# Kernel optimization log

Measured on AMD Instinct MI355X. Metric: run time of the kernel, lower is better.

The kernel has to match this reference:

```python
import jax, jax.numpy as jnp
import numpy as np

MID = 64        # conf.mid_channels
N_INV = 6       # n_layers=8 -> range(1, n_layers-1) -> 6 involution blocks
K = 7           # involution kernel size
GROUP_CH = 16   # RedNet default group_channels
GROUPS = MID // GROUP_CH   # 4
RED = MID // 4             # reduction_ratio = 4 -> 16


def conv2d(x, w, b=None, pad=0):
    out = jax.lax.conv_general_dilated(
        x, w, window_strides=(1, 1), padding=[(pad, pad), (pad, pad)],
        dimension_numbers=('NCHW', 'OIHW', 'NCHW'))
    if b is not None:
        out = out + b[None, :, None, None]
    return out


def extract_patches(x, k):
    # x: (B,C,H,W) -> (B,C,k*k,H,W), same-padded (torch nn.Unfold with pad=k//2)
    p = k // 2
    xp = jnp.pad(x, ((0, 0), (0, 0), (p, p), (p, p)))
    H, W = x.shape[2], x.shape[3]
    slices = [xp[:, :, i:i + H, j:j + W] for i in range(k) for j in range(k)]
    return jnp.stack(slices, axis=2)


def involution(x, red_w, bn_gamma, bn_beta, span_w, span_b):
    # kernel-generation branch: 1x1 conv (no bias) -> BN(eval, mean=0,var=1) -> ReLU -> 1x1 conv
    t = conv2d(x, red_w)                                     # (B,RED,H,W)
    t = bn_gamma[None, :, None, None] * t + bn_beta[None, :, None, None]
    t = jax.nn.relu(t)
    w = conv2d(t, span_w, span_b)                            # (B,K*K*GROUPS,H,W)
    B, _, H, W = w.shape
    w = w.reshape(B, GROUPS, K * K, H, W)
    patches = extract_patches(x, K).reshape(B, GROUPS, GROUP_CH, K * K, H, W)
    out = jnp.einsum('bgkhw,bgckhw->bgchw', w, patches)      # per-pixel dynamic conv
    return out.reshape(B, MID, H, W)


def setup_inputs() -> dict:
    key = jax.random.key(0)
    ks = jax.random.split(key, 12)
    s = 0.05
    inp = {
        'input_tensor': jax.random.normal(ks[0], (1, 3, 128, 128), jnp.float32),
        'conv_in_w': jax.random.normal(ks[1], (MID, 3, 3, 3), jnp.float32) * s,
        'conv_in_b': jax.random.normal(ks[2], (MID,), jnp.float32) * s,
        'red_w': jax.random.normal(ks[3], (N_INV, RED, MID, 1, 1), jnp.float32) * s,
        'bn_gamma': jnp.ones((N_INV, RED), jnp.float32),
        'bn_beta': jnp.zeros((N_INV, RED), jnp.float32),
        'span_w': jax.random.normal(ks[4], (N_INV, K * K * GROUPS, RED, 1, 1), jnp.float32) * s,
        'span_b': jax.random.normal(ks[5], (N_INV, K * K * GROUPS), jnp.float32) * s,
        'conv_out_w': jax.random.normal(ks[6], (12, MID, 3, 3), jnp.float32) * s,
        'conv_out_b': jax.random.normal(ks[7], (12,), jnp.float32) * s,
    }
    return inp


def reference(input_tensor, conv_in_w, conv_in_b, red_w, bn_gamma, bn_beta,
              span_w, span_b, conv_out_w, conv_out_b):
    x = conv2d(input_tensor, conv_in_w, conv_in_b, pad=2)     # (B,MID,H+2,W+2)
    for l in range(N_INV):
        x = jax.nn.relu(involution(x, red_w[l], bn_gamma[l], bn_beta[l],
                                   span_w[l], span_b[l]))
    pixel = conv2d(x, conv_out_w, conv_out_b, pad=0)          # (B,12,H,W)
    # PixelShuffle(2): (B,12,H,W) -> (B,3,2H,2W)
    B, _, H, W = pixel.shape
    out = pixel.reshape(B, 3, 2, 2, H, W).transpose(0, 1, 4, 2, 5, 3)
    return out.reshape(B, 3, 2 * H, 2 * W)
```

## Files before the change

kernel.cpp:

```cpp
#include <hip/hip_runtime.h>


#define HH 130
#define SP 136
#define PPL (SP*SP)
#define GP (PPL*16)
#define XBUF2 (4*GP)
#define TP1 (16900*16)
#define OFF_TA (2*XBUF2)
#define OFF_TB (OFF_TA + 4*TP1)

__global__ __launch_bounds__(256) void conv_in_kernel(
        const float* __restrict__ inf, const float* __restrict__ W,
        const float* __restrict__ b, float* __restrict__ x0,
        float* __restrict__ x1, float* __restrict__ tpA,
        const float* __restrict__ redw0) {
    const int tid = threadIdx.x;
    if (blockIdx.x >= 67) {
        int idx = ((blockIdx.x - 67)*4 + blockIdx.y)*256 + tid;
        if (idx < 3192) {
            int bsel = idx & 1, e = idx >> 1;
            int r, c;
            if (e < 816) { r = e/136; c = e%136; if (r >= 3) r += 130; }
            else { int j = e-816; r = 3 + j/6; int m = j%6; c = (m<3)? m : m+130; }
            float* base = (bsel ? x1 : x0) + ((size_t)r*SP + c)*16;
            float4 z = make_float4(0.f,0.f,0.f,0.f);
            #pragma unroll
            for (int g2 = 0; g2 < 4; ++g2)
                #pragma unroll
                for (int q = 0; q < 4; ++q)
                    *(float4*)(base + (size_t)g2*GP + q*4) = z;
        }
        return;
    }
    __shared__ float wl[448];
    const int g = blockIdx.y;
    for (int i = tid; i < 448; i += 256)
        wl[i] = (i < 432) ? W[g*432 + i] : b[g*16 + (i-432)];
    __syncthreads();
    int px = blockIdx.x*256 + tid;
    int pxc = px < 16900 ? px : 16899;
    int h = pxc/130, w = pxc%130;
    float xv[27];
    #pragma unroll
    for (int i = 0; i < 3; ++i)
      #pragma unroll
      for (int ky = 0; ky < 3; ++ky) {
        int y = h - 2 + ky;
        #pragma unroll
        for (int kx = 0; kx < 3; ++kx) {
            int xx = w - 2 + kx;
            float v = 0.f;
            if ((unsigned)y < 128u && (unsigned)xx < 128u)
                v = inf[i*16384 + y*128 + xx];
            xv[i*9 + ky*3 + kx] = v;
        }
      }
    float acc[16];
    #pragma unroll
    for (int c = 0; c < 16; ++c) {
        float a = wl[432 + c];
        #pragma unroll
        for (int t = 0; t < 27; ++t) a += wl[c*27 + t] * xv[t];
        acc[c] = a;
    }
    if (px < 16900) {
        float* dst = x0 + (size_t)g*GP + ((size_t)(h+3)*SP + (w+3))*16;
        #pragma unroll
        for (int q = 0; q < 4; ++q)
            *(float4*)(dst + q*4) =
                make_float4(acc[q*4], acc[q*4+1], acc[q*4+2], acc[q*4+3]);
        float* td = tpA + (size_t)g*TP1 + (size_t)px*16;
        #pragma unroll
        for (int rq = 0; rq < 4; ++rq) {
            float p0=0.f, p1=0.f, p2=0.f, p3=0.f;
            #pragma unroll
            for (int j = 0; j < 16; ++j) {
                float a = acc[j];
                p0 += redw0[(rq*4+0)*64 + g*16 + j]*a;
                p1 += redw0[(rq*4+1)*64 + g*16 + j]*a;
                p2 += redw0[(rq*4+2)*64 + g*16 + j]*a;
                p3 += redw0[(rq*4+3)*64 + g*16 + j]*a;
            }
            *(float4*)(td + rq*4) = make_float4(p0, p1, p2, p3);
        }
    }
}

#define TL(p, r)  uu[(p)*20 + (r)]
#define WLK(k, p) uu[(k)*68 + (p)]
__global__ __launch_bounds__(256, 5) void e_kernel(
        const float* __restrict__ x,
        const float* __restrict__ tread,
        float* __restrict__ twrite,
        const float* __restrict__ gamma, const float* __restrict__ beta,
        const float* __restrict__ spanw,
        const float* __restrict__ spanb,
        const float* __restrict__ redwn,
        float* __restrict__ xout,
        const int doNext)
{
    __shared__ float xl[4][14][17][4];
    __shared__ float uu[49*68];
    const int wid = blockIdx.x;
    const int slot = wid >> 3;
    const int T = (wid & 7)*37 + (slot >> 2);
    if (T >= 289) return;
    const int g = slot & 3;
    const int ty = (T/17)*8, tx = (T%17)*8;
    const int tid = threadIdx.x;
    const int px = tid & 63;
    const int wv = __builtin_amdgcn_readfirstlane(tid >> 6);
    const int sr = px >> 3, sc = px & 7;

    for (int i = tid; i < 784; i += 256) {
        int q = i & 3, p = i >> 2;
        int r = p / 14, c = p % 14;
        int gr = ty + r, gc = tx + c;
        gr = gr < SP ? gr : SP-1;
        gc = gc < SP ? gc : SP-1;
        float4 v = *(const float4*)(x + (size_t)g*GP
                                    + ((size_t)gr*SP + gc)*16 + q*4);
        *(float4*)&xl[q][r][c][0] = v;
    }

    const int hh = min(ty + sr, HH-1), ww = min(tx + sc, HH-1);
    {
        const size_t toff = ((size_t)hh*HH + ww)*16 + wv*4;
        float4 s = make_float4(0.f,0.f,0.f,0.f);
        #pragma unroll
        for (int gg = 0; gg < 4; ++gg) {
            float4 a = *(const float4*)(tread + (size_t)gg*TP1 + toff);
            s.x += a.x; s.y += a.y; s.z += a.z; s.w += a.w;
        }
        *(float4*)&TL(px, wv*4) = s;
    }
    __syncthreads();

    float t16[16];
    #pragma unroll
    for (int q = 0; q < 4; ++q) {
        float4 v = *(const float4*)&TL(px, q*4);
        t16[q*4+0] = fmaxf(gamma[q*4+0]*v.x + beta[q*4+0], 0.f);
        t16[q*4+1] = fmaxf(gamma[q*4+1]*v.y + beta[q*4+1], 0.f);
        t16[q*4+2] = fmaxf(gamma[q*4+2]*v.z + beta[q*4+2], 0.f);
        t16[q*4+3] = fmaxf(gamma[q*4+3]*v.w + beta[q*4+3], 0.f);
    }
    __syncthreads();

    {
        const float* sw = spanw + g*784;
        const float* sb = spanb + g*49;
        const int k0 = wv ? (wv*12 + 1) : 0;
        #pragma unroll
        for (int j = 0; j < 12; ++j) {
            int k = k0 + j;
            float a = sb[k];
            #pragma unroll
            for (int r = 0; r < 16; ++r) a += sw[k*16 + r] * t16[r];
            WLK(k, px) = a;
        }
        if (wv == 0) {
            float a = sb[12];
            #pragma unroll
            for (int r = 0; r < 16; ++r) a += sw[12*16 + r] * t16[r];
            WLK(12, px) = a;
        }
    }
    __syncthreads();

    float4 o0 = make_float4(0.f,0.f,0.f,0.f);
    float4 o1 = make_float4(0.f,0.f,0.f,0.f);
    int px0 = 0, cq2 = 0;
    if (tid < 128) {
        cq2 = tid >> 5;
        const int pr = tid & 31;
        const int sr2 = pr >> 2, sc0 = (pr & 3)*2;
        px0 = sr2*8 + sc0;
        float4 a0 = make_float4(0.f,0.f,0.f,0.f);
        float4 a1 = make_float4(0.f,0.f,0.f,0.f);
        #pragma unroll
        for (int i = 0; i < 7; ++i) {
            float4 row[8];
            #pragma unroll
            for (int j = 0; j < 8; ++j)
                row[j] = *(const float4*)&xl[cq2][sr2 + i][sc0 + j][0];
            #pragma unroll
            for (int j = 0; j < 7; ++j) {
                float2 wp = *(const float2*)&WLK(i*7 + j, px0);
                a0.x += wp.x*row[j].x;   a0.y += wp.x*row[j].y;
                a0.z += wp.x*row[j].z;   a0.w += wp.x*row[j].w;
                a1.x += wp.y*row[j+1].x; a1.y += wp.y*row[j+1].y;
                a1.z += wp.y*row[j+1].z; a1.w += wp.y*row[j+1].w;
            }
        }
        o0 = make_float4(fmaxf(a0.x,0.f), fmaxf(a0.y,0.f),
                         fmaxf(a0.z,0.f), fmaxf(a0.w,0.f));
        o1 = make_float4(fmaxf(a1.x,0.f), fmaxf(a1.y,0.f),
                         fmaxf(a1.z,0.f), fmaxf(a1.w,0.f));
        const int h2 = ty + sr2, w2 = tx + sc0;
        if (h2 < HH) {
            float* ob = xout + (size_t)g*GP
                        + ((size_t)(h2+3)*SP + (w2+3))*16 + cq2*4;
            if (w2 < HH)     *(float4*)ob        = o0;
            if (w2+1 < HH)   *(float4*)(ob + 16) = o1;
        }
    }

    if (doNext) {
        float* ol = (float*)xl;
        __syncthreads();
        if (tid < 128) {
            ol[ px0   *17 + cq2*4 + 0] = o0.x;
            ol[ px0   *17 + cq2*4 + 1] = o0.y;
            ol[ px0   *17 + cq2*4 + 2] = o0.z;
            ol[ px0   *17 + cq2*4 + 3] = o0.w;
            ol[(px0+1)*17 + cq2*4 + 0] = o1.x;
            ol[(px0+1)*17 + cq2*4 + 1] = o1.y;
            ol[(px0+1)*17 + cq2*4 + 2] = o1.z;
            ol[(px0+1)*17 + cq2*4 + 3] = o1.w;
        }
        __syncthreads();
        const int rq = wv;
        float p0=0.f, p1=0.f, p2=0.f, p3=0.f;
        #pragma unroll
        for (int j = 0; j < 16; ++j) {
            float xv = ol[px*17 + j];
            const int c = g*16 + j;
            p0 += redwn[(rq*4+0)*64 + c]*xv;
            p1 += redwn[(rq*4+1)*64 + c]*xv;
            p2 += redwn[(rq*4+2)*64 + c]*xv;
            p3 += redwn[(rq*4+3)*64 + c]*xv;
        }
        const int hR = ty + sr, wR = tx + sc;
        if (hR < HH && wR < HH)
            *(float4*)(twrite + (size_t)g*TP1
                       + ((size_t)hR*HH + wR)*16 + rq*4) =
                make_float4(p0, p1, p2, p3);
    }
}

__global__ __launch_bounds__(256) void conv_out_ps_kernel(
        const float* __restrict__ x, const float* __restrict__ W,
        const float* __restrict__ b, float* __restrict__ out)
{
    __shared__ float xh[64*120];
    __shared__ float wl[6912];
    const int tid = threadIdx.x;
    const int ty = blockIdx.y*8, tx = blockIdx.x*8;

    for (int idx = tid; idx < 6912; idx += 256) wl[idx] = W[idx];
    for (int idx = tid; idx < 1600; idx += 256) {
        int g = idx/400, rem = idx%400;
        int p100 = rem>>2, q = rem&3;
        int r = p100/10, cl = p100%10;
        float4 v = *(const float4*)(x + (size_t)g*GP
                     + ((size_t)(ty + r + 3)*SP + tx + cl + 3)*16 + q*4);
        int c0 = g*16 + q*4;
        xh[(c0+0)*120 + r*12 + cl] = v.x;
        xh[(c0+1)*120 + r*12 + cl] = v.y;
        xh[(c0+2)*120 + r*12 + cl] = v.z;
        xh[(c0+3)*120 + r*12 + cl] = v.w;
    }
    __syncthreads();

    const int wave = __builtin_amdgcn_readfirstlane(tid >> 6);
    const int lane = tid & 63;
    const int s = lane >> 2, cq = lane & 3;
    const int sr = s >> 1, pc0 = (s & 1)*4;
    float acc[3][4] = {};

    for (int c = cq*16; c < cq*16 + 16; ++c) {
        #pragma unroll
        for (int ky = 0; ky < 3; ++ky) {
            const float* xb = &xh[c*120 + (sr + ky)*12 + pc0];
            float4 xa = *(const float4*)xb;
            float2 xm = *(const float2*)(xb + 4);
            float xr[6] = {xa.x, xa.y, xa.z, xa.w, xm.x, xm.y};
            #pragma unroll
            for (int oj = 0; oj < 3; ++oj) {
                const float* wp = &wl[((wave*3 + oj)*64 + c)*9 + ky*3];
                #pragma unroll
                for (int kx = 0; kx < 3; ++kx) {
                    float wv = wp[kx];
                    #pragma unroll
                    for (int q = 0; q < 4; ++q)
                        acc[oj][q] += wv * xr[kx + q];
                }
            }
        }
    }

    #pragma unroll
    for (int oj = 0; oj < 3; ++oj)
        #pragma unroll
        for (int q = 0; q < 4; ++q) {
            float v = acc[oj][q];
            v += __shfl_xor(v, 1, 64);
            v += __shfl_xor(v, 2, 64);
            acc[oj][q] = v;
        }

    if (cq == 0) {
        #pragma unroll
        for (int oj = 0; oj < 3; ++oj) {
            int o = wave*3 + oj;
            float bo = b[o];
            int c3 = o >> 2, r = (o >> 1) & 1, s2 = o & 1;
            int h = ty + sr;
            #pragma unroll
            for (int q = 0; q < 4; ++q) {
                int w = tx + pc0 + q;
                out[c3*65536 + (2*h + r)*256 + 2*w + s2] = acc[oj][q] + bo;
            }
        }
    }
}

extern "C" void kernel_launch(void* const* d_in, const int* in_sizes, int n_in,
                              void* d_out, int out_size, void* d_ws, size_t ws_size,
                              hipStream_t stream) {
    const float* inf   = (const float*)d_in[0];
    const float* cinw  = (const float*)d_in[1];
    const float* cinb  = (const float*)d_in[2];
    const float* redw  = (const float*)d_in[3];
    const float* gam   = (const float*)d_in[4];
    const float* bet   = (const float*)d_in[5];
    const float* spw   = (const float*)d_in[6];
    const float* spb   = (const float*)d_in[7];
    const float* cow   = (const float*)d_in[8];
    const float* cob   = (const float*)d_in[9];

    float* ws = (float*)d_ws;
    float* x0 = ws;
    float* x1 = ws + XBUF2;
    float* tA = ws + OFF_TA;
    float* tB = ws + OFF_TB;

    conv_in_kernel<<<dim3(80, 4), 256, 0, stream>>>(
        inf, cinw, cinb, x0, x1, tA, redw);

    float* cur = x0; float* nxt = x1;
    for (int l = 0; l < 6; ++l) {
        const int doNext = (l < 5);
        float* tread  = (l & 1) ? tB : tA;
        float* twrite = (l & 1) ? tA : tB;
        e_kernel<<<1184, 256, 0, stream>>>(
            cur, tread, twrite,
            gam + l*16, bet + l*16,
            spw + l*3136, spb + l*196,
            redw + (doNext ? (l+1)*1024 : 0),
            nxt, doNext);
        float* t = cur; cur = nxt; nxt = t;
    }

    conv_out_ps_kernel<<<dim3(16, 16), 256, 0, stream>>>(
        cur, cow, cob, (float*)d_out);
}
```

Before: 175.3 us.

## Enlarge involution tile to 16x8 pixels per block with all threads computing

After: 218.7 us. 24.7% more time.

```diff
diff --git a/kernel.cpp b/kernel.cpp
--- a/kernel.cpp
+++ b/kernel.cpp
@@ -88,8 +88,8 @@
 }
 
 #define TL(p, r)  uu[(p)*20 + (r)]
-#define WLK(k, p) uu[(k)*68 + (p)]
-__global__ __launch_bounds__(256, 5) void e_kernel(
+#define WLK(k, p) uu[(k)*132 + (p)]
+__global__ __launch_bounds__(256, 3) void e_kernel(
         const float* __restrict__ x,
         const float* __restrict__ tread,
         float* __restrict__ twrite,
@@ -100,20 +100,18 @@
         float* __restrict__ xout,
         const int doNext)
 {
-    __shared__ float xl[4][14][17][4];
-    __shared__ float uu[49*68];
+    __shared__ float xl[4][22][17][4];
+    __shared__ float uu[49*132];
     const int wid = blockIdx.x;
-    const int slot = wid >> 3;
-    const int T = (wid & 7)*37 + (slot >> 2);
-    if (T >= 289) return;
-    const int g = slot & 3;
-    const int ty = (T/17)*8, tx = (T%17)*8;
+    const int g = wid & 3;
+    const int T = wid >> 2;
+    const int ty = (T/17)*16, tx = (T%17)*8;
     const int tid = threadIdx.x;
-    const int px = tid & 63;
-    const int wv = __builtin_amdgcn_readfirstlane(tid >> 6);
-    const int sr = px >> 3, sc = px & 7;
-
-    for (int i = tid; i < 784; i += 256) {
+    const int px2 = tid & 127;
+    const int hf = __builtin_amdgcn_readfirstlane(tid >> 7);
+    const int sr = px2 >> 3, sc = px2 & 7;
+
+    for (int i = tid; i < 1232; i += 256) {
         int q = i & 3, p = i >> 2;
         int r = p / 14, c = p % 14;
         int gr = ty + r, gc = tx + c;
@@ -126,21 +124,25 @@
 
     const int hh = min(ty + sr, HH-1), ww = min(tx + sc, HH-1);
     {
-        const size_t toff = ((size_t)hh*HH + ww)*16 + wv*4;
-        float4 s = make_float4(0.f,0.f,0.f,0.f);
+        const size_t toff = ((size_t)hh*HH + ww)*16 + hf*8;
+        float4 s0 = make_float4(0.f,0.f,0.f,0.f);
+        float4 s1 = make_float4(0.f,0.f,0.f,0.f);
         #pragma unroll
         for (int gg = 0; gg < 4; ++gg) {
             float4 a = *(const float4*)(tread + (size_t)gg*TP1 + toff);
-            s.x += a.x; s.y += a.y; s.z += a.z; s.w += a.w;
-        }
-        *(float4*)&TL(px, wv*4) = s;
+            float4 b = *(const float4*)(tread + (size_t)gg*TP1 + toff + 4);
+            s0.x += a.x; s0.y += a.y; s0.z += a.z; s0.w += a.w;
+            s1.x += b.x; s1.y += b.y; s1.z += b.z; s1.w += b.w;
+        }
+        *(float4*)&TL(px2, hf*8)     = s0;
+        *(float4*)&TL(px2, hf*8 + 4) = s1;
     }
     __syncthreads();
 
     float t16[16];
     #pragma unroll
     for (int q = 0; q < 4; ++q) {
-        float4 v = *(const float4*)&TL(px, q*4);
+        float4 v = *(const float4*)&TL(px2, q*4);
         t16[q*4+0] = fmaxf(gamma[q*4+0]*v.x + beta[q*4+0], 0.f);
         t16[q*4+1] = fmaxf(gamma[q*4+1]*v.y + beta[q*4+1], 0.f);
         t16[q*4+2] = fmaxf(gamma[q*4+2]*v.z + beta[q*4+2], 0.f);
@@ -151,92 +153,87 @@
     {
         const float* sw = spanw + g*784;
         const float* sb = spanb + g*49;
-        const int k0 = wv ? (wv*12 + 1) : 0;
-        #pragma unroll
-        for (int j = 0; j < 12; ++j) {
+        const int k0 = hf*25;
+        #pragma unroll
+        for (int j = 0; j < 25; ++j) {
             int k = k0 + j;
-            float a = sb[k];
-            #pragma unroll
-            for (int r = 0; r < 16; ++r) a += sw[k*16 + r] * t16[r];
-            WLK(k, px) = a;
-        }
-        if (wv == 0) {
-            float a = sb[12];
-            #pragma unroll
-            for (int r = 0; r < 16; ++r) a += sw[12*16 + r] * t16[r];
-            WLK(12, px) = a;
-        }
-    }
-    __syncthreads();
-
-    float4 o0 = make_float4(0.f,0.f,0.f,0.f);
-    float4 o1 = make_float4(0.f,0.f,0.f,0.f);
-    int px0 = 0, cq2 = 0;
-    if (tid < 128) {
-        cq2 = tid >> 5;
-        const int pr = tid & 31;
-        const int sr2 = pr >> 2, sc0 = (pr & 3)*2;
-        px0 = sr2*8 + sc0;
-        float4 a0 = make_float4(0.f,0.f,0.f,0.f);
-        float4 a1 = make_float4(0.f,0.f,0.f,0.f);
-        #pragma unroll
-        for (int i = 0; i < 7; ++i) {
-            float4 row[8];
-            #pragma unroll
-            for (int j = 0; j < 8; ++j)
-                row[j] = *(const float4*)&xl[cq2][sr2 + i][sc0 + j][0];
-            #pragma unroll
-            for (int j = 0; j < 7; ++j) {
-                float2 wp = *(const float2*)&WLK(i*7 + j, px0);
-                a0.x += wp.x*row[j].x;   a0.y += wp.x*row[j].y;
-                a0.z += wp.x*row[j].z;   a0.w += wp.x*row[j].w;
-                a1.x += wp.y*row[j+1].x; a1.y += wp.y*row[j+1].y;
-                a1.z += wp.y*row[j+1].z; a1.w += wp.y*row[j+1].w;
+            if (k < 49) {
+                float a = sb[k];
+                #pragma unroll
+                for (int r = 0; r < 16; ++r) a += sw[k*16 + r] * t16[r];
+                WLK(k, px2) = a;
             }
         }
-        o0 = make_float4(fmaxf(a0.x,0.f), fmaxf(a0.y,0.f),
-                         fmaxf(a0.z,0.f), fmaxf(a0.w,0.f));
-        o1 = make_float4(fmaxf(a1.x,0.f), fmaxf(a1.y,0.f),
-                         fmaxf(a1.z,0.f), fmaxf(a1.w,0.f));
-        const int h2 = ty + sr2, w2 = tx + sc0;
-        if (h2 < HH) {
-            float* ob = xout + (size_t)g*GP
-                        + ((size_t)(h2+3)*SP + (w2+3))*16 + cq2*4;
-            if (w2 < HH)     *(float4*)ob        = o0;
-            if (w2+1 < HH)   *(float4*)(ob + 16) = o1;
-        }
+    }
+    __syncthreads();
+
+    const int cq2 = __builtin_amdgcn_readfirstlane(tid >> 6);
+    const int p = tid & 63;
+    const int sr2 = p >> 2, sc0 = (p & 3)*2;
+    const int px0 = sr2*8 + sc0;
+    float4 a0 = make_float4(0.f,0.f,0.f,0.f);
+    float4 a1 = make_float4(0.f,0.f,0.f,0.f);
+    #pragma unroll
+    for (int i = 0; i < 7; ++i) {
+        float4 row[8];
+        #pragma unroll
+        for (int j = 0; j < 8; ++j)
+            row[j] = *(const float4*)&xl[cq2][sr2 + i][sc0 + j][0];
+        #pragma unroll
+        for (int j = 0; j < 7; ++j) {
+            float2 wp = *(const float2*)&WLK(i*7 + j, px0);
+            a0.x += wp.x*row[j].x;   a0.y += wp.x*row[j].y;
+            a0.z += wp.x*row[j].z;   a0.w += wp.x*row[j].w;
+            a1.x += wp.y*row[j+1].x; a1.y += wp.y*row[j+1].y;
+            a1.z += wp.y*row[j+1].z; a1.w += wp.y*row[j+1].w;
+        }
+    }
+    float4 o0 = make_float4(fmaxf(a0.x,0.f), fmaxf(a0.y,0.f),
+                            fmaxf(a0.z,0.f), fmaxf(a0.w,0.f));
+    float4 o1 = make_float4(fmaxf(a1.x,0.f), fmaxf(a1.y,0.f),
+                            fmaxf(a1.z,0.f), fmaxf(a1.w,0.f));
+    const int h2 = ty + sr2, w2 = tx + sc0;
+    if (h2 < HH) {
+        float* ob = xout + (size_t)g*GP
+                    + ((size_t)(h2+3)*SP + (w2+3))*16 + cq2*4;
+        if (w2 < HH)     *(float4*)ob        = o0;
+        if (w2+1 < HH)   *(float4*)(ob + 16) = o1;
     }
 
     if (doNext) {
         float* ol = (float*)xl;
         __syncthreads();
-        if (tid < 128) {
-            ol[ px0   *17 + cq2*4 + 0] = o0.x;
-            ol[ px0   *17 + cq2*4 + 1] = o0.y;
-            ol[ px0   *17 + cq2*4 + 2] = o0.z;
-            ol[ px0   *17 + cq2*4 + 3] = o0.w;
-            ol[(px0+1)*17 + cq2*4 + 0] = o1.x;
-            ol[(px0+1)*17 + cq2*4 + 1] = o1.y;
-            ol[(px0+1)*17 + cq2*4 + 2] = o1.z;
-            ol[(px0+1)*17 + cq2*4 + 3] = o1.w;
-        }
+        ol[ px0   *17 + cq2*4 + 0] = o0.x;
+        ol[ px0   *17 + cq2*4 + 1] = o0.y;
+        ol[ px0   *17 + cq2*4 + 2] = o0.z;
+        ol[ px0   *17 + cq2*4 + 3] = o0.w;
+        ol[(px0+1)*17 + cq2*4 + 0] = o1.x;
+        ol[(px0+1)*17 + cq2*4 + 1] = o1.y;
+        ol[(px0+1)*17 + cq2*4 + 2] = o1.z;
+        ol[(px0+1)*17 + cq2*4 + 3] = o1.w;
         __syncthreads();
-        const int rq = wv;
-        float p0=0.f, p1=0.f, p2=0.f, p3=0.f;
+        float p0=0.f, p1=0.f, p2v=0.f, p3=0.f;
+        float p4=0.f, p5=0.f, p6=0.f, p7=0.f;
         #pragma unroll
         for (int j = 0; j < 16; ++j) {
-            float xv = ol[px*17 + j];
+            float xv = ol[px2*17 + j];
             const int c = g*16 + j;
-            p0 += redwn[(rq*4+0)*64 + c]*xv;
-            p1 += redwn[(rq*4+1)*64 + c]*xv;
-            p2 += redwn[(rq*4+2)*64 + c]*xv;
-            p3 += redwn[(rq*4+3)*64 + c]*xv;
+            p0 += redwn[(hf*8+0)*64 + c]*xv;
+            p1 += redwn[(hf*8+1)*64 + c]*xv;
+            p2v+= redwn[(hf*8+2)*64 + c]*xv;
+            p3 += redwn[(hf*8+3)*64 + c]*xv;
+            p4 += redwn[(hf*8+4)*64 + c]*xv;
+            p5 += redwn[(hf*8+5)*64 + c]*xv;
+            p6 += redwn[(hf*8+6)*64 + c]*xv;
+            p7 += redwn[(hf*8+7)*64 + c]*xv;
         }
         const int hR = ty + sr, wR = tx + sc;
-        if (hR < HH && wR < HH)
-            *(float4*)(twrite + (size_t)g*TP1
-                       + ((size_t)hR*HH + wR)*16 + rq*4) =
-                make_float4(p0, p1, p2, p3);
+        if (hR < HH && wR < HH) {
+            float* tb = twrite + (size_t)g*TP1
+                        + ((size_t)hR*HH + wR)*16 + hf*8;
+            *(float4*)tb       = make_float4(p0, p1, p2v, p3);
+            *(float4*)(tb + 4) = make_float4(p4, p5, p6, p7);
+        }
     }
 }
 
@@ -345,7 +342,7 @@
         const int doNext = (l < 5);
         float* tread  = (l & 1) ? tB : tA;
         float* twrite = (l & 1) ? tA : tB;
-        e_kernel<<<1184, 256, 0, stream>>>(
+        e_kernel<<<612, 256, 0, stream>>>(
             cur, tread, twrite,
             gam + l*16, bet + l*16,
             spw + l*3136, spb + l*196,
```
